# Kernel optimization log

Hardware: AMD Instinct MI355X
Metric: run time of the kernel (lower is better)

## Reference

```python
import jax, jax.numpy as jnp
import numpy as np
import math

B, L, D, H, F = 4, 2048, 1024, 16, 4096
SF = 5          # sampling_factor
EPS = 1e-12     # LayerNorm eps


def setup_inputs() -> dict:
    key = jax.random.key(0)
    ks = jax.random.split(key, 18)
    s = 0.02
    lin = lambda k, i, o: (jax.random.normal(k, (i, o), jnp.float32) * s)
    log_LK = math.ceil(math.log1p(L))
    U_part = min(SF * L * log_LK, L)  # = L here
    return {
        "x": jax.random.normal(ks[0], (B, L, D), jnp.float32),
        "wq": lin(ks[1], D, D), "bq": jnp.zeros((D,), jnp.float32),
        "wk": lin(ks[2], D, D), "bk": jnp.zeros((D,), jnp.float32),
        "wv": lin(ks[3], D, D), "bv": jnp.zeros((D,), jnp.float32),
        "wo": lin(ks[4], D, D), "bo": jnp.zeros((D,), jnp.float32),
        "w1": lin(ks[5], D, F), "b1": jnp.zeros((F,), jnp.float32),
        "w2": lin(ks[6], F, D), "b2": jnp.zeros((D,), jnp.float32),
        "gamma1": jnp.ones((D,), jnp.float32), "beta1": jnp.zeros((D,), jnp.float32),
        "gamma2": jnp.ones((D,), jnp.float32), "beta2": jnp.zeros((D,), jnp.float32),
        "index_sample": jax.random.randint(ks[7], (U_part,), 0, L, jnp.int32),
    }


def _layernorm(x, g, b):
    m = x.mean(-1, keepdims=True)
    v = ((x - m) ** 2).mean(-1, keepdims=True)  # unbiased=False
    return g * (x - m) / jnp.sqrt(v + EPS) + b


def _prob_sparse_mha(x, wq, bq, wk, bk, wv, bv, wo, bo, index_sample):
    d = D // H
    BH = B * H
    # NOTE: source views q as (B, H, L, d) WITHOUT transpose (quirk kept);
    # k, v are split with the usual (B, L, H, d) -> (B, H, L, d) transpose.
    q = (x @ wq + bq).reshape(BH, L, d)
    k = (x @ wk + bk).reshape(B, L, H, d).transpose(0, 2, 1, 3).reshape(BH, L, d)
    v = (x @ wv + bv).reshape(B, L, H, d).transpose(0, 2, 1, 3).reshape(BH, L, d)

    # --- ProbSparse query selection ---
    K_sample = k[:, index_sample, :]                       # [BH, U_part, d]
    QK = jnp.einsum('bqd,bkd->bqk', q, K_sample)           # [BH, L, U_part]
    M = QK.max(axis=-1) - QK.sum(axis=-1) / L              # sparsity measure
    u = min(SF * math.ceil(math.log1p(L)), L)              # static: 40
    _, M_top = jax.lax.top_k(-M, u)                        # largest=False in src
    Q_reduce = jnp.take_along_axis(q, M_top[:, :, None], axis=1)  # [BH, u, d]

    # --- attention for the selected queries ---
    scores = jnp.einsum('bud,bkd->buk', Q_reduce, k) / math.sqrt(d)
    probs = jax.nn.softmax(scores, axis=-1)
    out_red = jnp.einsum('buk,bkd->bud', probs, v)         # [BH, u, d]

    # scatter reduced outputs back to full length (non-selected rows -> 0)
    full = jnp.zeros_like(q).at[jnp.arange(BH)[:, None], M_top].set(out_red)
    out = full.reshape(B, H, L, d).transpose(0, 2, 1, 3).reshape(B, L, D)
    return out @ wo + bo


def reference(x, wq, bq, wk, bk, wv, bv, wo, bo, w1, b1, w2, b2,
              gamma1, beta1, gamma2, beta2, index_sample):
    a = _prob_sparse_mha(x, wq, bq, wk, bk, wv, bv, wo, bo, index_sample)
    x1 = _layernorm(x + a, gamma1, beta1)          # dropout = identity (eval)
    f = jnp.maximum(x1 @ w1 + b1, 0.0) @ w2 + b2   # FFN (ReLU)
    return _layernorm(x1 + f, gamma2, beta2)
```

## Files before the change

### kernel.cpp

```cpp
#include <hip/hip_runtime.h>
#include <float.h>
#include <math.h>

#define L_SEQ 2048
#define D_MODEL 1024
#define N_HEAD 16
#define HD 64
#define N_BH 64
#define U_TOP 40

using bf16x8 = __attribute__((ext_vector_type(8))) short;
using f32x4  = __attribute__((ext_vector_type(4))) float;

__device__ __forceinline__ unsigned short f2bf(float f) {
    unsigned int u = __builtin_bit_cast(unsigned int, f);
    u += 0x7fff + ((u >> 16) & 1);
    return (unsigned short)(u >> 16);
}
__device__ __forceinline__ float bf2f(unsigned short h) {
    unsigned int u = ((unsigned int)h) << 16;
    return __builtin_bit_cast(float, u);
}

__device__ __forceinline__ void gload_lds16(const void* g, void* l) {
    __builtin_amdgcn_global_load_lds(
        (const __attribute__((address_space(1))) unsigned int*)g,
        (__attribute__((address_space(3))) unsigned int*)l, 16, 0, 0);
}

template<bool OUTBF16, bool RELU, bool ACCUM>
__global__ void __launch_bounds__(256)
gemm_bf16(const unsigned short* __restrict__ A, int lda,
          const unsigned short* __restrict__ BT, int ldbt,
          void* __restrict__ Cp, int ldc, int K,
          const float* __restrict__ bias)
{
    __shared__ short As[4096];
    __shared__ short Bs[4096];
    const int tid = threadIdx.x;
    const int w = tid >> 6, l = tid & 63;
    const int bx = blockIdx.x, by = blockIdx.y;
    const int wm = w >> 1, wn = w & 1;

    f32x4 acc[4][4] = {};

    const unsigned short* a_src[2];
    const unsigned short* b_src[2];
#pragma unroll
    for (int g = 0; g < 2; ++g) {
        int r = w * 32 + g * 16 + (l >> 2);
        int kc = (l & 3) ^ ((r >> 1) & 3);
        a_src[g] = A + (size_t)(by * 128 + r) * lda + kc * 8;
        b_src[g] = BT + (size_t)(bx * 128 + r) * ldbt + kc * 8;
    }
    short* As_w = As + w * 1024;
    short* Bs_w = Bs + w * 1024;

    const int lr = l & 15, lg = l >> 4;

    for (int k0 = 0; k0 < K; k0 += 32) {
        __syncthreads();
        gload_lds16(a_src[0] + k0, As_w);
        gload_lds16(a_src[1] + k0, As_w + 512);
        gload_lds16(b_src[0] + k0, Bs_w);
        gload_lds16(b_src[1] + k0, Bs_w + 512);
        __syncthreads();

        bf16x8 af[4], bg[4];
#pragma unroll
        for (int m = 0; m < 4; ++m) {
            int row = wm * 64 + m * 16 + lr;
            int off = row * 64 + ((lg ^ ((row >> 1) & 3)) << 4);
            af[m] = *(const bf16x8*)((const char*)As + off);
        }
#pragma unroll
        for (int n = 0; n < 4; ++n) {
            int row = wn * 64 + n * 16 + lr;
            int off = row * 64 + ((lg ^ ((row >> 1) & 3)) << 4);
            bg[n] = *(const bf16x8*)((const char*)Bs + off);
        }
#pragma unroll
        for (int m = 0; m < 4; ++m)
#pragma unroll
            for (int n = 0; n < 4; ++n)
                acc[m][n] = __builtin_amdgcn_mfma_f32_16x16x32_bf16(
                    af[m], bg[n], acc[m][n], 0, 0, 0);
    }

    float bcol[4];
#pragma unroll
    for (int n = 0; n < 4; ++n) {
        int colg = bx * 128 + wn * 64 + n * 16 + lr;
        bcol[n] = bias ? bias[colg] : 0.f;
    }
#pragma unroll
    for (int m = 0; m < 4; ++m) {
#pragma unroll
        for (int n = 0; n < 4; ++n) {
            int colg = bx * 128 + wn * 64 + n * 16 + lr;
#pragma unroll
            for (int r = 0; r < 4; ++r) {
                int rowg = by * 128 + wm * 64 + m * 16 + lg * 4 + r;
                float v = acc[m][n][r] + bcol[n];
                if (RELU) v = fmaxf(v, 0.f);
                if (OUTBF16) {
                    ((unsigned short*)Cp)[(size_t)rowg * ldc + colg] = f2bf(v);
                } else {
                    float* C = (float*)Cp;
                    if (ACCUM) v += C[(size_t)rowg * ldc + colg];
                    C[(size_t)rowg * ldc + colg] = v;
                }
            }
        }
    }
}

__global__ void __launch_bounds__(256)
gemm_bf16_split(const unsigned short* __restrict__ Ah,
                const unsigned short* __restrict__ Al, int lda,
                const unsigned short* __restrict__ BhT,
                const unsigned short* __restrict__ BlT, int ldbt,
                unsigned short* __restrict__ Ch,
                unsigned short* __restrict__ Cl, int ldc, int K,
                const float* __restrict__ bias)
{
    __shared__ short Ash[4096], Asl[4096], Bsh[4096], Bsl[4096];
    const int tid = threadIdx.x;
    const int w = tid >> 6, l = tid & 63;
    const int bx = blockIdx.x, by = blockIdx.y;
    const int wm = w >> 1, wn = w & 1;

    f32x4 acc[4][4] = {};

    size_t a_off[2], b_off[2];
#pragma unroll
    for (int g = 0; g < 2; ++g) {
        int r = w * 32 + g * 16 + (l >> 2);
        int kc = (l & 3) ^ ((r >> 1) & 3);
        a_off[g] = (size_t)(by * 128 + r) * lda + kc * 8;
        b_off[g] = (size_t)(bx * 128 + r) * ldbt + kc * 8;
    }
    const int wb = w * 1024;
    const int lr = l & 15, lg = l >> 4;

    for (int k0 = 0; k0 < K; k0 += 32) {
        __syncthreads();
#pragma unroll
        for (int g = 0; g < 2; ++g) {
            gload_lds16(Ah + a_off[g] + k0, Ash + wb + g * 512);
            gload_lds16(Al + a_off[g] + k0, Asl + wb + g * 512);
            gload_lds16(BhT + b_off[g] + k0, Bsh + wb + g * 512);
            gload_lds16(BlT + b_off[g] + k0, Bsl + wb + g * 512);
        }
        __syncthreads();

        bf16x8 afh[4], afl[4], bgh[4], bgl[4];
#pragma unroll
        for (int m = 0; m < 4; ++m) {
            int row = wm * 64 + m * 16 + lr;
            int off = row * 64 + ((lg ^ ((row >> 1) & 3)) << 4);
            afh[m] = *(const bf16x8*)((const char*)Ash + off);
            afl[m] = *(const bf16x8*)((const char*)Asl + off);
        }
#pragma unroll
        for (int n = 0; n < 4; ++n) {
            int row = wn * 64 + n * 16 + lr;
            int off = row * 64 + ((lg ^ ((row >> 1) & 3)) << 4);
            bgh[n] = *(const bf16x8*)((const char*)Bsh + off);
            bgl[n] = *(const bf16x8*)((const char*)Bsl + off);
        }
#pragma unroll
        for (int m = 0; m < 4; ++m)
#pragma unroll
            for (int n = 0; n < 4; ++n) {
                acc[m][n] = __builtin_amdgcn_mfma_f32_16x16x32_bf16(
                    afh[m], bgh[n], acc[m][n], 0, 0, 0);
                acc[m][n] = __builtin_amdgcn_mfma_f32_16x16x32_bf16(
                    afh[m], bgl[n], acc[m][n], 0, 0, 0);
                acc[m][n] = __builtin_amdgcn_mfma_f32_16x16x32_bf16(
                    afl[m], bgh[n], acc[m][n], 0, 0, 0);
            }
    }

    float bcol[4];
#pragma unroll
    for (int n = 0; n < 4; ++n)
        bcol[n] = bias[bx * 128 + wn * 64 + n * 16 + lr];
#pragma unroll
    for (int m = 0; m < 4; ++m)
#pragma unroll
        for (int n = 0; n < 4; ++n) {
            int colg = bx * 128 + wn * 64 + n * 16 + lr;
#pragma unroll
            for (int r = 0; r < 4; ++r) {
                int rowg = by * 128 + wm * 64 + m * 16 + lg * 4 + r;
                float v = acc[m][n][r] + bcol[n];
                unsigned short hh = f2bf(v);
                unsigned short ll = f2bf(v - bf2f(hh));
                Ch[(size_t)rowg * ldc + colg] = hh;
                Cl[(size_t)rowg * ldc + colg] = ll;
            }
        }
}

__global__ void __launch_bounds__(256)
mstat_mfma(const unsigned short* __restrict__ Qh, const unsigned short* __restrict__ Ql,
           const unsigned short* __restrict__ Kh, const unsigned short* __restrict__ Kl,
           const int* __restrict__ idxs, float* __restrict__ Mout)
{
    __shared__ short Qs[2][8192];
    __shared__ short Ks[2][4096];
    const int tid = threadIdx.x, w = tid >> 6, l = tid & 63;
    const int itile = blockIdx.x, bh = blockIdx.y;
    const int b = bh >> 4, h = bh & 15;
    const int i0 = itile * 128;
    const int lr = l & 15, lg = l >> 4;

#pragma unroll
    for (int g = w * 4; g < w * 4 + 4; ++g) {
        int row = g * 8 + (l >> 3);
        int kc = (l & 7) ^ (row & 7);
        size_t src = (size_t)(bh * L_SEQ + i0 + row) * HD + kc * 8;
        gload_lds16(Qh + src, (char*)&Qs[0][0] + g * 1024);
        gload_lds16(Ql + src, (char*)&Qs[1][0] + g * 1024);
    }
    __syncthreads();

    bf16x8 af[2][2][2];
#pragma unroll
    for (int m = 0; m < 2; ++m) {
        int row = (w * 2 + m) * 16 + lr;
#pragma unroll
        for (int k = 0; k < 2; ++k) {
            int c = k * 4 + lg;
            int off = row * 128 + ((c ^ (row & 7)) << 4);
            af[m][k][0] = *(const bf16x8*)((const char*)&Qs[0][0] + off);
            af[m][k][1] = *(const bf16x8*)((const char*)&Qs[1][0] + off);
        }
    }

    float mx[2][4], sm[2][4];
#pragma unroll
    for (int m = 0; m < 2; ++m)
#pragma unroll
        for (int r = 0; r < 4; ++r) { mx[m][r] = -FLT_MAX; sm[m][r] = 0.f; }

    for (int jt = 0; jt < 32; ++jt) {
        const int j0 = jt * 64;
        __syncthreads();
#pragma unroll
        for (int g = 2 * w; g <= 2 * w + 1; ++g) {
            int row = g * 8 + (l >> 3);
            int kc = (l & 7) ^ (row & 7);
            int gr = idxs[j0 + row];
            size_t src = (size_t)(b * L_SEQ + gr) * D_MODEL + h * HD + kc * 8;
            gload_lds16(Kh + src, (char*)&Ks[0][0] + g * 1024);
            gload_lds16(Kl + src, (char*)&Ks[1][0] + g * 1024);
        }
        __syncthreads();

        bf16x8 bgh[4][2], bgl[4][2];
#pragma unroll
        for (int n = 0; n < 4; ++n) {
            int row = n * 16 + lr;
#pragma unroll
            for (int k = 0; k < 2; ++k) {
                int c = k * 4 + lg;
                int off = row * 128 + ((c ^ (row & 7)) << 4);
                bgh[n][k] = *(const bf16x8*)((const char*)&Ks[0][0] + off);
                bgl[n][k] = *(const bf16x8*)((const char*)&Ks[1][0] + off);
            }
        }
#pragma unroll
        for (int m = 0; m < 2; ++m) {
            f32x4 a0[4];
#pragma unroll
            for (int n = 0; n < 4; ++n) {
                f32x4 a = {};
                a = __builtin_amdgcn_mfma_f32_16x16x32_bf16(af[m][0][0], bgh[n][0], a, 0, 0, 0);
                a = __builtin_amdgcn_mfma_f32_16x16x32_bf16(af[m][0][0], bgl[n][0], a, 0, 0, 0);
                a = __builtin_amdgcn_mfma_f32_16x16x32_bf16(af[m][0][1], bgh[n][0], a, 0, 0, 0);
                a = __builtin_amdgcn_mfma_f32_16x16x32_bf16(af[m][1][0], bgh[n][1], a, 0, 0, 0);
                a = __builtin_amdgcn_mfma_f32_16x16x32_bf16(af[m][1][0], bgl[n][1], a, 0, 0, 0);
                a = __builtin_amdgcn_mfma_f32_16x16x32_bf16(af[m][1][1], bgh[n][1], a, 0, 0, 0);
                a0[n] = a;
            }
#pragma unroll
            for (int r = 0; r < 4; ++r) {
                float vmax = fmaxf(fmaxf(a0[0][r], a0[1][r]), fmaxf(a0[2][r], a0[3][r]));
                float vsum = (a0[0][r] + a0[1][r]) + (a0[2][r] + a0[3][r]);
                mx[m][r] = fmaxf(mx[m][r], vmax);
                sm[m][r] += vsum;
            }
        }
    }

#pragma unroll
    for (int m = 0; m < 2; ++m)
#pragma unroll
        for (int r = 0; r < 4; ++r) {
            float a = mx[m][r], s = sm[m][r];
#pragma unroll
            for (int mask = 1; mask < 16; mask <<= 1) {
                a = fmaxf(a, __shfl_xor(a, mask));
                s += __shfl_xor(s, mask);
            }
            if (lr == 0) {
                int row = i0 + (w * 2 + m) * 16 + lg * 4 + r;
                Mout[(size_t)bh * L_SEQ + row] = a - s * (1.0f / 2048.0f);
            }
        }
}

__global__ void __launch_bounds__(256)
tconv(const float* __restrict__ in, int R, int C, unsigned short* __restrict__ out)
{
    __shared__ float t[32][33];
    const int bx = blockIdx.x * 32;
    const int by = blockIdx.y * 32;
    const int lx = threadIdx.x & 31, ly = threadIdx.x >> 5;
#pragma unroll
    for (int r = 0; r < 4; ++r)
        t[ly + r * 8][lx] = in[(size_t)(by + ly + r * 8) * C + bx + lx];
    __syncthreads();
#pragma unroll
    for (int r = 0; r < 4; ++r) {
        int oc = ly + r * 8;
        out[(size_t)(bx + oc) * R + by + lx] = f2bf(t[lx][oc]);
    }
}

__global__ void __launch_bounds__(256)
tconv_split(const float* __restrict__ in, int R, int C,
            unsigned short* __restrict__ outh, unsigned short* __restrict__ outl)
{
    __shared__ float t[32][33];
    const int bx = blockIdx.x * 32;
    const int by = blockIdx.y * 32;
    const int lx = threadIdx.x & 31, ly = threadIdx.x >> 5;
#pragma unroll
    for (int r = 0; r < 4; ++r)
        t[ly + r * 8][lx] = in[(size_t)(by + ly + r * 8) * C + bx + lx];
    __syncthreads();
#pragma unroll
    for (int r = 0; r < 4; ++r) {
        int oc = ly + r * 8;
        float f = t[lx][oc];
        unsigned short hh = f2bf(f);
        outh[(size_t)(bx + oc) * R + by + lx] = hh;
        outl[(size_t)(bx + oc) * R + by + lx] = f2bf(f - bf2f(hh));
    }
}

__global__ void __launch_bounds__(256)
split_f32(const float* __restrict__ in, unsigned short* __restrict__ hi,
          unsigned short* __restrict__ lo)
{
    size_t i = ((size_t)blockIdx.x * 256 + threadIdx.x) * 4;
    float4 v = *(const float4*)(in + i);
    ushort4 h, l2;
    h.x = f2bf(v.x); l2.x = f2bf(v.x - bf2f(h.x));
    h.y = f2bf(v.y); l2.y = f2bf(v.y - bf2f(h.y));
    h.z = f2bf(v.z); l2.z = f2bf(v.z - bf2f(h.z));
    h.w = f2bf(v.w); l2.w = f2bf(v.w - bf2f(h.w));
    *(ushort4*)(hi + i) = h;
    *(ushort4*)(lo + i) = l2;
}

__global__ void __launch_bounds__(256)
topk_kernel(const float* __restrict__ M, int* __restrict__ Mtop)
{
    __shared__ float mv[L_SEQ];
    __shared__ float wv_[4];
    __shared__ int wi_[4];
    const int bh = blockIdx.x;
    const int tid = threadIdx.x;
    for (int j = tid; j < L_SEQ; j += 256) mv[j] = M[(size_t)bh * L_SEQ + j];
    __syncthreads();
    for (int u = 0; u < U_TOP; ++u) {
        float best = FLT_MAX;
        int bi = 1 << 30;
        for (int j = tid; j < L_SEQ; j += 256) {
            float v = mv[j];
            if (v < best || (v == best && j < bi)) { best = v; bi = j; }
        }
#pragma unroll
        for (int off = 32; off; off >>= 1) {
            float ov = __shfl_down(best, off);
            int oi = __shfl_down(bi, off);
            if (ov < best || (ov == best && oi < bi)) { best = ov; bi = oi; }
        }
        if ((tid & 63) == 0) { wv_[tid >> 6] = best; wi_[tid >> 6] = bi; }
        __syncthreads();
        if (tid == 0) {
            for (int w = 1; w < 4; ++w)
                if (wv_[w] < best || (wv_[w] == best && wi_[w] < bi)) { best = wv_[w]; bi = wi_[w]; }
            Mtop[bh * U_TOP + u] = bi;
            mv[bi] = FLT_MAX;
        }
        __syncthreads();
    }
}

__global__ void __launch_bounds__(256)
attn_fused(const unsigned short* __restrict__ Q,
           const unsigned short* __restrict__ K,
           const unsigned short* __restrict__ V,
           const int* __restrict__ Mtop,
           unsigned short* __restrict__ ATT)
{
    __shared__ unsigned short Qs[64 * 64];
    __shared__ unsigned short Ks[128 * 64];
    __shared__ unsigned short Vt[64 * 128];
    __shared__ unsigned short Pb[64 * 128];
    const int bh = blockIdx.x;
    const int b = bh >> 4, h = bh & 15;
    const int tid = threadIdx.x, w = tid >> 6, l = tid & 63;
    const int lr = l & 15, lg = l >> 4;

#pragma unroll
    for (int is = 0; is < 2; ++is) {
        int row = w * 16 + is * 8 + (l >> 3);
        int u = row < U_TOP ? row : U_TOP - 1;
        int lsel = Mtop[bh * U_TOP + u];
        int cg = (l & 7) ^ (row & 7);
        gload_lds16(Q + (((size_t)(bh * L_SEQ + lsel)) << 6) + cg * 8,
                    &Qs[(w * 16 + is * 8) * 64]);
    }
    __syncthreads();

    bf16x8 af[2];
    {
        int row = w * 16 + lr;
#pragma unroll
        for (int ks = 0; ks < 2; ++ks) {
            int c = (ks * 4 + lg) ^ (row & 7);
            af[ks] = *(const bf16x8*)((const char*)Qs + row * 128 + (c << 4));
        }
    }

    float m_run[4], l_run[4];
    f32x4 oacc[4] = {};
#pragma unroll
    for (int r = 0; r < 4; ++r) { m_run[r] = -FLT_MAX; l_run[r] = 0.f; }

    for (int t = 0; t < 16; ++t) {
        const int j0 = t * 128;
        __syncthreads();

#pragma unroll
        for (int is = 0; is < 4; ++is) {
            int kr = w * 32 + is * 8 + (l >> 3);
            int cg = (l & 7) ^ (kr & 7);
            gload_lds16(K + (((size_t)(b * L_SEQ + j0 + kr)) << 10) + (h << 6) + cg * 8,
                        &Ks[(w * 32 + is * 8) * 64]);
        }
        {
            int key = tid & 127, dh = (tid >> 7) * 32;
            const unsigned short* vsrc =
                V + (((size_t)(b * L_SEQ + j0 + key)) << 10) + (h << 6) + dh;
            bf16x8 vv[4];
#pragma unroll
            for (int i = 0; i < 4; ++i) vv[i] = *(const bf16x8*)(vsrc + i * 8);
            int ck = key >> 3, klo = (key & 7) * 2;
#pragma unroll
            for (int i = 0; i < 4; ++i)
#pragma unroll
                for (int j = 0; j < 8; ++j) {
                    int d = dh + i * 8 + j;
                    *(unsigned short*)((char*)Vt + d * 256 +
                                       ((ck ^ (d & 7)) << 4) + klo) =
                        (unsigned short)vv[i][j];
                }
        }
        __syncthreads();

        f32x4 sc[8] = {};
#pragma unroll
        for (int ks = 0; ks < 2; ++ks)
#pragma unroll
            for (int n = 0; n < 8; ++n) {
                int krow = n * 16 + lr;
                int c = (ks * 4 + lg) ^ (krow & 7);
                bf16x8 bf = *(const bf16x8*)((const char*)Ks + krow * 128 + (c << 4));
                sc[n] = __builtin_amdgcn_mfma_f32_16x16x32_bf16(af[ks], bf, sc[n], 0, 0, 0);
            }

        float rs[4];
#pragma unroll
        for (int r = 0; r < 4; ++r) {
            int row = w * 16 + lg * 4 + r;
            float mt = -FLT_MAX;
#pragma unroll
            for (int n = 0; n < 8; ++n) mt = fmaxf(mt, sc[n][r]);
            mt *= 0.125f;
#pragma unroll
            for (int mask = 1; mask < 16; mask <<= 1)
                mt = fmaxf(mt, __shfl_xor(mt, mask));
            float mn = fmaxf(m_run[r], mt);
            rs[r] = expf(m_run[r] - mn);
            float ls = 0.f;
            int rsw = row & 7;
#pragma unroll
            for (int n = 0; n < 8; ++n) {
                float p = expf(sc[n][r] * 0.125f - mn);
                ls += p;
                int ckp = (lr >> 3) + 2 * n;
                *(unsigned short*)((char*)Pb + row * 256 +
                                   ((ckp ^ rsw) << 4) + (lr & 7) * 2) = f2bf(p);
            }
#pragma unroll
            for (int mask = 1; mask < 16; mask <<= 1) ls += __shfl_xor(ls, mask);
            l_run[r] = l_run[r] * rs[r] + ls;
            m_run[r] = mn;
        }
        __syncthreads();

#pragma unroll
        for (int n = 0; n < 4; ++n)
#pragma unroll
            for (int r = 0; r < 4; ++r) oacc[n][r] *= rs[r];
#pragma unroll
        for (int ks = 0; ks < 4; ++ks) {
            int arow = w * 16 + lr;
            int ca = (lg + ks * 4) ^ (arow & 7);
            bf16x8 pa = *(const bf16x8*)((const char*)Pb + arow * 256 + (ca << 4));
#pragma unroll
            for (int n = 0; n < 4; ++n) {
                int d = n * 16 + lr;
                int cb = (lg + ks * 4) ^ (d & 7);
                bf16x8 vb = *(const bf16x8*)((const char*)Vt + d * 256 + (cb << 4));
                oacc[n] = __builtin_amdgcn_mfma_f32_16x16x32_bf16(pa, vb, oacc[n], 0, 0, 0);
            }
        }
    }

#pragma unroll
    for (int r = 0; r < 4; ++r) {
        int row = w * 16 + lg * 4 + r;
        if (row < U_TOP) {
            int lsel = Mtop[bh * U_TOP + row];
            float inv = 1.f / l_run[r];
            size_t base = (((size_t)(b * L_SEQ + lsel)) << 10) + (h << 6);
#pragma unroll
            for (int n = 0; n < 4; ++n)
                ATT[base + n * 16 + lr] = f2bf(oacc[n][r] * inv);
        }
    }
}

template<bool WB16>
__global__ void __launch_bounds__(256)
ln_kernel(const float* __restrict__ X, const float* __restrict__ A,
          const float* __restrict__ g, const float* __restrict__ be,
          float* __restrict__ out, unsigned short* __restrict__ out16)
{
    __shared__ float wred[4];
    const int row = blockIdx.x, tid = threadIdx.x;
    float4 xv = *(const float4*)(X + (size_t)row * D_MODEL + tid * 4);
    float4 av = *(const float4*)(A + (size_t)row * D_MODEL + tid * 4);
    float v0 = xv.x + av.x, v1 = xv.y + av.y, v2 = xv.z + av.z, v3 = xv.w + av.w;

    float s = v0 + v1 + v2 + v3;
#pragma unroll
    for (int off = 32; off; off >>= 1) s += __shfl_down(s, off);
    if ((tid & 63) == 0) wred[tid >> 6] = s;
    __syncthreads();
    float mean = (wred[0] + wred[1] + wred[2] + wred[3]) * (1.f / 1024.f);
    __syncthreads();

    float d0 = v0 - mean, d1 = v1 - mean, d2 = v2 - mean, d3 = v3 - mean;
    float q = d0 * d0 + d1 * d1 + d2 * d2 + d3 * d3;
#pragma unroll
    for (int off = 32; off; off >>= 1) q += __shfl_down(q, off);
    if ((tid & 63) == 0) wred[tid >> 6] = q;
    __syncthreads();
    float var = (wred[0] + wred[1] + wred[2] + wred[3]) * (1.f / 1024.f);
    float rstd = rsqrtf(var + 1e-12f);

    float4 gv = *(const float4*)(g + tid * 4);
    float4 bv = *(const float4*)(be + tid * 4);
    float4 o;
    o.x = gv.x * d0 * rstd + bv.x;
    o.y = gv.y * d1 * rstd + bv.y;
    o.z = gv.z * d2 * rstd + bv.z;
    o.w = gv.w * d3 * rstd + bv.w;
    *(float4*)(out + (size_t)row * D_MODEL + tid * 4) = o;
    if (WB16) {
        ushort4 ob;
        ob.x = f2bf(o.x); ob.y = f2bf(o.y); ob.z = f2bf(o.z); ob.w = f2bf(o.w);
        *(ushort4*)(out16 + (size_t)row * D_MODEL + tid * 4) = ob;
    }
}

extern "C" void kernel_launch(void* const* d_in, const int* in_sizes, int n_in,
                              void* d_out, int out_size, void* d_ws, size_t ws_size,
                              hipStream_t stream)
{
    const float* x   = (const float*)d_in[0];
    const float* wq  = (const float*)d_in[1];
    const float* bq  = (const float*)d_in[2];
    const float* wk  = (const float*)d_in[3];
    const float* bk  = (const float*)d_in[4];
    const float* wv  = (const float*)d_in[5];
    const float* bv  = (const float*)d_in[6];
    const float* wo  = (const float*)d_in[7];
    const float* bo  = (const float*)d_in[8];
    const float* w1  = (const float*)d_in[9];
    const float* b1  = (const float*)d_in[10];
    const float* w2  = (const float*)d_in[11];
    const float* b2  = (const float*)d_in[12];
    const float* g1  = (const float*)d_in[13];
    const float* be1 = (const float*)d_in[14];
    const float* g2  = (const float*)d_in[15];
    const float* be2 = (const float*)d_in[16];
    const int*  idxs = (const int*)d_in[17];

    char* ws = (char*)d_ws;
    const size_t MB = 1u << 20;
    unsigned short* Qhb  = (unsigned short*)(ws);
    unsigned short* Qlb  = (unsigned short*)(ws + 16 * MB);
    unsigned short* Khb  = (unsigned short*)(ws + 32 * MB);
    unsigned short* Klb  = (unsigned short*)(ws + 48 * MB);
    unsigned short* xh   = (unsigned short*)(ws + 64 * MB);
    unsigned short* xl   = (unsigned short*)(ws + 80 * MB);
    unsigned short* ATTb = (unsigned short*)(ws + 64 * MB);
    unsigned short* x1b  = (unsigned short*)(ws + 80 * MB);
    unsigned short* wqhT = (unsigned short*)(ws + 96 * MB);
    unsigned short* wqlT = (unsigned short*)(ws + 98 * MB);
    unsigned short* wkhT = (unsigned short*)(ws + 100 * MB);
    unsigned short* wklT = (unsigned short*)(ws + 102 * MB);
    unsigned short* wvT  = (unsigned short*)(ws + 104 * MB);
    unsigned short* woT  = (unsigned short*)(ws + 106 * MB);
    float* Mb            = (float*)(ws + 96 * MB);
    int*   Mtop          = (int*)(ws + 97 * MB);
    unsigned short* Vb   = (unsigned short*)(ws + 108 * MB);
    float* Ab            = (float*)(ws);
    float* x1f           = (float*)(ws + 32 * MB);
    unsigned short* w1T  = (unsigned short*)(ws + 96 * MB);
    unsigned short* w2T  = (unsigned short*)(ws + 104 * MB);
    unsigned short* HIDc = (unsigned short*)(ws);
    float* F             = (float*)d_out;

    dim3 blk(256);
    dim3 g_gemm(8, 64);

    split_f32<<<dim3(8192), blk, 0, stream>>>(x, xh, xl);
    tconv_split<<<dim3(32, 32), blk, 0, stream>>>(wq, 1024, 1024, wqhT, wqlT);
    tconv_split<<<dim3(32, 32), blk, 0, stream>>>(wk, 1024, 1024, wkhT, wklT);
    tconv<<<dim3(32, 32), blk, 0, stream>>>(wv, 1024, 1024, wvT);
    tconv<<<dim3(32, 32), blk, 0, stream>>>(wo, 1024, 1024, woT);

    gemm_bf16_split<<<g_gemm, blk, 0, stream>>>(xh, xl, 1024, wqhT, wqlT, 1024,
                                                Qhb, Qlb, 1024, 1024, bq);
    gemm_bf16_split<<<g_gemm, blk, 0, stream>>>(xh, xl, 1024, wkhT, wklT, 1024,
                                                Khb, Klb, 1024, 1024, bk);
    gemm_bf16<true, false, false><<<g_gemm, blk, 0, stream>>>(xh, 1024, wvT, 1024,
                                                              Vb, 1024, 1024, bv);

    mstat_mfma<<<dim3(16, 64), blk, 0, stream>>>(Qhb, Qlb, Khb, Klb, idxs, Mb);
    topk_kernel<<<dim3(64), blk, 0, stream>>>(Mb, Mtop);

    hipMemsetAsync(ATTb, 0, 16 * MB, stream);
    attn_fused<<<dim3(N_BH), blk, 0, stream>>>(Qhb, Khb, Vb, Mtop, ATTb);

    gemm_bf16<false, false, false><<<g_gemm, blk, 0, stream>>>(ATTb, 1024, woT, 1024,
                                                               Ab, 1024, 1024, bo);
    ln_kernel<true><<<dim3(8192), blk, 0, stream>>>(x, Ab, g1, be1, x1f, x1b);

    tconv<<<dim3(128, 32), blk, 0, stream>>>(w1, 1024, 4096, w1T);
    tconv<<<dim3(32, 128), blk, 0, stream>>>(w2, 4096, 1024, w2T);

    for (int c = 0; c < 2; ++c) {
        gemm_bf16<true, true, false><<<dim3(16, 64), blk, 0, stream>>>(
            x1b, 1024, w1T + (size_t)c * 2048 * 1024, 1024, HIDc, 2048, 1024, b1 + c * 2048);
        if (c == 0)
            gemm_bf16<false, false, false><<<g_gemm, blk, 0, stream>>>(
                HIDc, 2048, w2T + c * 2048, 4096, F, 1024, 2048, b2);
        else
            gemm_bf16<false, false, true><<<g_gemm, blk, 0, stream>>>(
                HIDc, 2048, w2T + c * 2048, 4096, F, 1024, 2048, nullptr);
    }

    ln_kernel<false><<<dim3(8192), blk, 0, stream>>>(x1f, F, g2, be2, (float*)d_out, nullptr);
}
```

Before: 862.1 us.

## Exploit sparse attention output: scatter-project via Wo, pack Q/K hi-lo, pre-gather K samples

Replaces the dense attention-output GEMM with a small kernel that multiplies only the 40 selected rows per head by the Wo slice and atomically adds into a zeroed buffer, with the bias moved into the LayerNorm. This skips a full 8192x1024x1024 GEMM on mostly-zero rows. Q and K hi/lo halves are now interleaved in one packed layout, and the sampled K rows are gathered once into a contiguous buffer so the M-statistic kernel can double-buffer plain loads with larger query tiles. Atomics make the summation order nondeterministic, and several buffers now live in the output region.

```diff
diff --git a/kernel.cpp b/kernel.cpp
--- a/kernel.cpp
+++ b/kernel.cpp
@@ -120,8 +120,7 @@
                 const unsigned short* __restrict__ Al, int lda,
                 const unsigned short* __restrict__ BhT,
                 const unsigned short* __restrict__ BlT, int ldbt,
-                unsigned short* __restrict__ Ch,
-                unsigned short* __restrict__ Cl, int ldc, int K,
+                unsigned short* __restrict__ CP, int K,
                 const float* __restrict__ bias)
 {
     __shared__ short Ash[4096], Asl[4096], Bsh[4096], Bsl[4096];
@@ -186,117 +185,134 @@
 #pragma unroll
     for (int n = 0; n < 4; ++n)
         bcol[n] = bias[bx * 128 + wn * 64 + n * 16 + lr];
+    const int cg = bx * 2 + wn;
 #pragma unroll
     for (int m = 0; m < 4; ++m)
 #pragma unroll
         for (int n = 0; n < 4; ++n) {
-            int colg = bx * 128 + wn * 64 + n * 16 + lr;
+            int cwi = n * 16 + lr;
 #pragma unroll
             for (int r = 0; r < 4; ++r) {
                 int rowg = by * 128 + wm * 64 + m * 16 + lg * 4 + r;
                 float v = acc[m][n][r] + bcol[n];
                 unsigned short hh = f2bf(v);
                 unsigned short ll = f2bf(v - bf2f(hh));
-                Ch[(size_t)rowg * ldc + colg] = hh;
-                Cl[(size_t)rowg * ldc + colg] = ll;
-            }
-        }
-}
-
-__global__ void __launch_bounds__(256)
-mstat_mfma(const unsigned short* __restrict__ Qh, const unsigned short* __restrict__ Ql,
-           const unsigned short* __restrict__ Kh, const unsigned short* __restrict__ Kl,
-           const int* __restrict__ idxs, float* __restrict__ Mout)
-{
-    __shared__ short Qs[2][8192];
-    __shared__ short Ks[2][4096];
+                size_t ad = (size_t)rowg * 2048 + cg * 128 + cwi;
+                CP[ad] = hh;
+                CP[ad + 64] = ll;
+            }
+        }
+}
+
+__global__ void __launch_bounds__(256)
+gather_ks(const unsigned short* __restrict__ KP, const int* __restrict__ idxs,
+          unsigned short* __restrict__ KS)
+{
+    const int bh = blockIdx.x, b = bh >> 4, h = bh & 15;
+    const int r0 = blockIdx.y * 256;
+    const int s = threadIdx.x & 15, jr = threadIdx.x >> 4;
+#pragma unroll
+    for (int p = 0; p < 16; ++p) {
+        int j = r0 + p * 16 + jr;
+        int idx = idxs[j];
+        int kc = (s & 7) ^ (j & 7);
+        const unsigned short* src = KP + (size_t)(b * 2048 + idx) * 2048
+                                  + h * 128 + ((s & 8) << 3) + kc * 8;
+        *(bf16x8*)(KS + ((size_t)bh * 2048 + j) * 128 + s * 8) =
+            *(const bf16x8*)src;
+    }
+}
+
+__global__ void __launch_bounds__(256)
+mstat_mfma2(const unsigned short* __restrict__ QP,
+            const unsigned short* __restrict__ KS,
+            float* __restrict__ Mout)
+{
+    __shared__ char lds[32768];
     const int tid = threadIdx.x, w = tid >> 6, l = tid & 63;
-    const int itile = blockIdx.x, bh = blockIdx.y;
-    const int b = bh >> 4, h = bh & 15;
-    const int i0 = itile * 128;
+    const int bh = blockIdx.x, qt = blockIdx.y;
+    const int i0 = qt * 256;
     const int lr = l & 15, lg = l >> 4;
 
-#pragma unroll
-    for (int g = w * 4; g < w * 4 + 4; ++g) {
-        int row = g * 8 + (l >> 3);
-        int kc = (l & 7) ^ (row & 7);
-        size_t src = (size_t)(bh * L_SEQ + i0 + row) * HD + kc * 8;
-        gload_lds16(Qh + src, (char*)&Qs[0][0] + g * 1024);
-        gload_lds16(Ql + src, (char*)&Qs[1][0] + g * 1024);
+    bf16x8 af[4][2][2];
+#pragma unroll
+    for (int half = 0; half < 2; ++half) {
+        __syncthreads();
+#pragma unroll
+        for (int it = 0; it < 8; ++it) {
+            int rq = w * 64 + it * 8 + (l >> 3);
+            int i = i0 + rq;
+            int kc = (l & 7) ^ (rq & 7);
+            gload_lds16(QP + (size_t)(bh * 128 + (i >> 4)) * 2048
+                           + (i & 15) * 128 + half * 64 + kc * 8,
+                        lds + w * 8192 + it * 1024);
+        }
+        __syncthreads();
+#pragma unroll
+        for (int m = 0; m < 4; ++m) {
+            int rq = w * 64 + m * 16 + lr;
+#pragma unroll
+            for (int ks = 0; ks < 2; ++ks) {
+                int c = (ks * 4 + lg) ^ (rq & 7);
+                af[m][ks][half] = *(const bf16x8*)(lds + rq * 128 + (c << 4));
+            }
+        }
     }
     __syncthreads();
 
-    bf16x8 af[2][2][2];
-#pragma unroll
-    for (int m = 0; m < 2; ++m) {
-        int row = (w * 2 + m) * 16 + lr;
-#pragma unroll
-        for (int k = 0; k < 2; ++k) {
-            int c = k * 4 + lg;
-            int off = row * 128 + ((c ^ (row & 7)) << 4);
-            af[m][k][0] = *(const bf16x8*)((const char*)&Qs[0][0] + off);
-            af[m][k][1] = *(const bf16x8*)((const char*)&Qs[1][0] + off);
-        }
-    }
-
-    float mx[2][4], sm[2][4];
-#pragma unroll
-    for (int m = 0; m < 2; ++m)
+    float mx[4][4], sm[4][4];
+#pragma unroll
+    for (int m = 0; m < 4; ++m)
 #pragma unroll
         for (int r = 0; r < 4; ++r) { mx[m][r] = -FLT_MAX; sm[m][r] = 0.f; }
 
+    const unsigned short* ksbase = KS + (size_t)bh * (2048 * 128);
+
+#pragma unroll
+    for (int it = 0; it < 4; ++it)
+        gload_lds16(ksbase + w * 2048 + it * 512 + l * 8,
+                    lds + w * 4096 + it * 1024);
+
     for (int jt = 0; jt < 32; ++jt) {
-        const int j0 = jt * 64;
-        __syncthreads();
-#pragma unroll
-        for (int g = 2 * w; g <= 2 * w + 1; ++g) {
-            int row = g * 8 + (l >> 3);
-            int kc = (l & 7) ^ (row & 7);
-            int gr = idxs[j0 + row];
-            size_t src = (size_t)(b * L_SEQ + gr) * D_MODEL + h * HD + kc * 8;
-            gload_lds16(Kh + src, (char*)&Ks[0][0] + g * 1024);
-            gload_lds16(Kl + src, (char*)&Ks[1][0] + g * 1024);
-        }
-        __syncthreads();
-
-        bf16x8 bgh[4][2], bgl[4][2];
+        const int cur = jt & 1;
+        __syncthreads();
+        if (jt + 1 < 32) {
+#pragma unroll
+            for (int it = 0; it < 4; ++it)
+                gload_lds16(ksbase + (size_t)(jt + 1) * 8192 + w * 2048 + it * 512 + l * 8,
+                            lds + (cur ^ 1) * 16384 + w * 4096 + it * 1024);
+        }
+        const char* kb = lds + cur * 16384;
 #pragma unroll
         for (int n = 0; n < 4; ++n) {
-            int row = n * 16 + lr;
-#pragma unroll
-            for (int k = 0; k < 2; ++k) {
-                int c = k * 4 + lg;
-                int off = row * 128 + ((c ^ (row & 7)) << 4);
-                bgh[n][k] = *(const bf16x8*)((const char*)&Ks[0][0] + off);
-                bgl[n][k] = *(const bf16x8*)((const char*)&Ks[1][0] + off);
-            }
-        }
-#pragma unroll
-        for (int m = 0; m < 2; ++m) {
-            f32x4 a0[4];
-#pragma unroll
-            for (int n = 0; n < 4; ++n) {
+            int jr = n * 16 + lr;
+            bf16x8 bgh[2], bgl[2];
+#pragma unroll
+            for (int ks = 0; ks < 2; ++ks) {
+                int c = (ks * 4 + lg) ^ (jr & 7);
+                bgh[ks] = *(const bf16x8*)(kb + jr * 256 + (c << 4));
+                bgl[ks] = *(const bf16x8*)(kb + jr * 256 + (c << 4) + 128);
+            }
+#pragma unroll
+            for (int m = 0; m < 4; ++m) {
                 f32x4 a = {};
-                a = __builtin_amdgcn_mfma_f32_16x16x32_bf16(af[m][0][0], bgh[n][0], a, 0, 0, 0);
-                a = __builtin_amdgcn_mfma_f32_16x16x32_bf16(af[m][0][0], bgl[n][0], a, 0, 0, 0);
-                a = __builtin_amdgcn_mfma_f32_16x16x32_bf16(af[m][0][1], bgh[n][0], a, 0, 0, 0);
-                a = __builtin_amdgcn_mfma_f32_16x16x32_bf16(af[m][1][0], bgh[n][1], a, 0, 0, 0);
-                a = __builtin_amdgcn_mfma_f32_16x16x32_bf16(af[m][1][0], bgl[n][1], a, 0, 0, 0);
-                a = __builtin_amdgcn_mfma_f32_16x16x32_bf16(af[m][1][1], bgh[n][1], a, 0, 0, 0);
-                a0[n] = a;
-            }
-#pragma unroll
-            for (int r = 0; r < 4; ++r) {
-                float vmax = fmaxf(fmaxf(a0[0][r], a0[1][r]), fmaxf(a0[2][r], a0[3][r]));
-                float vsum = (a0[0][r] + a0[1][r]) + (a0[2][r] + a0[3][r]);
-                mx[m][r] = fmaxf(mx[m][r], vmax);
-                sm[m][r] += vsum;
-            }
-        }
-    }
-
-#pragma unroll
-    for (int m = 0; m < 2; ++m)
+                a = __builtin_amdgcn_mfma_f32_16x16x32_bf16(af[m][0][0], bgh[0], a, 0, 0, 0);
+                a = __builtin_amdgcn_mfma_f32_16x16x32_bf16(af[m][0][1], bgh[0], a, 0, 0, 0);
+                a = __builtin_amdgcn_mfma_f32_16x16x32_bf16(af[m][0][0], bgl[0], a, 0, 0, 0);
+                a = __builtin_amdgcn_mfma_f32_16x16x32_bf16(af[m][1][0], bgh[1], a, 0, 0, 0);
+                a = __builtin_amdgcn_mfma_f32_16x16x32_bf16(af[m][1][1], bgh[1], a, 0, 0, 0);
+                a = __builtin_amdgcn_mfma_f32_16x16x32_bf16(af[m][1][0], bgl[1], a, 0, 0, 0);
+#pragma unroll
+                for (int r = 0; r < 4; ++r) {
+                    mx[m][r] = fmaxf(mx[m][r], a[r]);
+                    sm[m][r] += a[r];
+                }
+            }
+        }
+    }
+
+#pragma unroll
+    for (int m = 0; m < 4; ++m)
 #pragma unroll
         for (int r = 0; r < 4; ++r) {
             float a = mx[m][r], s = sm[m][r];
@@ -306,7 +322,7 @@
                 s += __shfl_xor(s, mask);
             }
             if (lr == 0) {
-                int row = i0 + (w * 2 + m) * 16 + lg * 4 + r;
+                int row = i0 + w * 64 + m * 16 + lg * 4 + r;
                 Mout[(size_t)bh * L_SEQ + row] = a - s * (1.0f / 2048.0f);
             }
         }
@@ -403,11 +419,11 @@
 }
 
 __global__ void __launch_bounds__(256)
-attn_fused(const unsigned short* __restrict__ Q,
-           const unsigned short* __restrict__ K,
+attn_fused(const unsigned short* __restrict__ QP,
+           const unsigned short* __restrict__ KP,
            const unsigned short* __restrict__ V,
            const int* __restrict__ Mtop,
-           unsigned short* __restrict__ ATT)
+           unsigned short* __restrict__ OUTC)
 {
     __shared__ unsigned short Qs[64 * 64];
     __shared__ unsigned short Ks[128 * 64];
@@ -424,7 +440,8 @@
         int u = row < U_TOP ? row : U_TOP - 1;
         int lsel = Mtop[bh * U_TOP + u];
         int cg = (l & 7) ^ (row & 7);
-        gload_lds16(Q + (((size_t)(bh * L_SEQ + lsel)) << 6) + cg * 8,
+        gload_lds16(QP + (size_t)(bh * 128 + (lsel >> 4)) * 2048
+                       + (lsel & 15) * 128 + cg * 8,
                     &Qs[(w * 16 + is * 8) * 64]);
     }
     __syncthreads();
@@ -452,7 +469,7 @@
         for (int is = 0; is < 4; ++is) {
             int kr = w * 32 + is * 8 + (l >> 3);
             int cg = (l & 7) ^ (kr & 7);
-            gload_lds16(K + (((size_t)(b * L_SEQ + j0 + kr)) << 10) + (h << 6) + cg * 8,
+            gload_lds16(KP + (size_t)(b * 2048 + j0 + kr) * 2048 + h * 128 + cg * 8,
                         &Ks[(w * 32 + is * 8) * 64]);
         }
         {
@@ -538,20 +555,66 @@
 #pragma unroll
     for (int r = 0; r < 4; ++r) {
         int row = w * 16 + lg * 4 + r;
-        if (row < U_TOP) {
-            int lsel = Mtop[bh * U_TOP + row];
-            float inv = 1.f / l_run[r];
-            size_t base = (((size_t)(b * L_SEQ + lsel)) << 10) + (h << 6);
-#pragma unroll
-            for (int n = 0; n < 4; ++n)
-                ATT[base + n * 16 + lr] = f2bf(oacc[n][r] * inv);
-        }
-    }
-}
-
-template<bool WB16>
+        float inv = 1.f / l_run[r];
+#pragma unroll
+        for (int n = 0; n < 4; ++n)
+            OUTC[bh * 4096 + row * 64 + n * 16 + lr] = f2bf(oacc[n][r] * inv);
+    }
+}
+
+__global__ void __launch_bounds__(256)
+woscatter(const unsigned short* __restrict__ OUTC,
+          const unsigned short* __restrict__ woT,
+          const int* __restrict__ Mtop,
+          float* __restrict__ Ab)
+{
+    const int bh = blockIdx.x, b = bh >> 4, h = bh & 15;
+    const int tid = threadIdx.x, w = tid >> 6, l = tid & 63;
+    const int lr = l & 15, lg = l >> 4;
+
+    bf16x8 af[3][2];
+#pragma unroll
+    for (int m = 0; m < 3; ++m)
+#pragma unroll
+        for (int ks = 0; ks < 2; ++ks)
+            af[m][ks] = *(const bf16x8*)(OUTC + bh * 4096 + (m * 16 + lr) * 64
+                                         + (ks * 4 + lg) * 8);
+    int lsel[3][4];
+#pragma unroll
+    for (int m = 0; m < 3; ++m)
+#pragma unroll
+        for (int r = 0; r < 4; ++r) {
+            int row = m * 16 + lg * 4 + r;
+            lsel[m][r] = row < U_TOP ? Mtop[bh * U_TOP + row] : -1;
+        }
+
+    for (int nn = 0; nn < 16; ++nn) {
+        int ng = w * 16 + nn;
+        bf16x8 bg[2];
+#pragma unroll
+        for (int ks = 0; ks < 2; ++ks)
+            bg[ks] = *(const bf16x8*)(woT + (size_t)(ng * 16 + lr) * 1024
+                                      + h * 64 + (ks * 4 + lg) * 8);
+        f32x4 a[3] = {};
+#pragma unroll
+        for (int m = 0; m < 3; ++m)
+#pragma unroll
+            for (int ks = 0; ks < 2; ++ks)
+                a[m] = __builtin_amdgcn_mfma_f32_16x16x32_bf16(af[m][ks], bg[ks], a[m], 0, 0, 0);
+#pragma unroll
+        for (int m = 0; m < 3; ++m)
+#pragma unroll
+            for (int r = 0; r < 4; ++r)
+                if (lsel[m][r] >= 0)
+                    atomicAdd(Ab + (size_t)(b * 2048 + lsel[m][r]) * 1024
+                              + ng * 16 + lr, a[m][r]);
+    }
+}
+
+template<bool WB16, bool BADD>
 __global__ void __launch_bounds__(256)
 ln_kernel(const float* __restrict__ X, const float* __restrict__ A,
+          const float* __restrict__ badd,
           const float* __restrict__ g, const float* __restrict__ be,
           float* __restrict__ out, unsigned short* __restrict__ out16)
 {
@@ -560,6 +623,10 @@
     float4 xv = *(const float4*)(X + (size_t)row * D_MODEL + tid * 4);
     float4 av = *(const float4*)(A + (size_t)row * D_MODEL + tid * 4);
     float v0 = xv.x + av.x, v1 = xv.y + av.y, v2 = xv.z + av.z, v3 = xv.w + av.w;
+    if (BADD) {
+        float4 bb = *(const float4*)(badd + tid * 4);
+        v0 += bb.x; v1 += bb.y; v2 += bb.z; v3 += bb.w;
+    }
 
     float s = v0 + v1 + v2 + v3;
 #pragma unroll
@@ -616,31 +683,33 @@
     const float* be2 = (const float*)d_in[16];
     const int*  idxs = (const int*)d_in[17];
 
-    char* ws = (char*)d_ws;
+    char* ws  = (char*)d_ws;
+    char* dob = (char*)d_out;
     const size_t MB = 1u << 20;
-    unsigned short* Qhb  = (unsigned short*)(ws);
-    unsigned short* Qlb  = (unsigned short*)(ws + 16 * MB);
-    unsigned short* Khb  = (unsigned short*)(ws + 32 * MB);
-    unsigned short* Klb  = (unsigned short*)(ws + 48 * MB);
+
+    unsigned short* QP   = (unsigned short*)(ws);
+    unsigned short* KP   = (unsigned short*)(ws + 32 * MB);
     unsigned short* xh   = (unsigned short*)(ws + 64 * MB);
     unsigned short* xl   = (unsigned short*)(ws + 80 * MB);
-    unsigned short* ATTb = (unsigned short*)(ws + 64 * MB);
-    unsigned short* x1b  = (unsigned short*)(ws + 80 * MB);
-    unsigned short* wqhT = (unsigned short*)(ws + 96 * MB);
-    unsigned short* wqlT = (unsigned short*)(ws + 98 * MB);
-    unsigned short* wkhT = (unsigned short*)(ws + 100 * MB);
-    unsigned short* wklT = (unsigned short*)(ws + 102 * MB);
-    unsigned short* wvT  = (unsigned short*)(ws + 104 * MB);
-    unsigned short* woT  = (unsigned short*)(ws + 106 * MB);
-    float* Mb            = (float*)(ws + 96 * MB);
-    int*   Mtop          = (int*)(ws + 97 * MB);
-    unsigned short* Vb   = (unsigned short*)(ws + 108 * MB);
-    float* Ab            = (float*)(ws);
-    float* x1f           = (float*)(ws + 32 * MB);
-    unsigned short* w1T  = (unsigned short*)(ws + 96 * MB);
-    unsigned short* w2T  = (unsigned short*)(ws + 104 * MB);
-    unsigned short* HIDc = (unsigned short*)(ws);
-    float* F             = (float*)d_out;
+    unsigned short* KS   = (unsigned short*)(ws + 64 * MB);
+    float*          Ab   = (float*)(ws + 64 * MB);
+    float*          x1f  = (float*)(ws + 96 * MB);
+    unsigned short* x1b  = (unsigned short*)(ws);
+    unsigned short* w1T  = (unsigned short*)(ws + 16 * MB);
+    unsigned short* w2T  = (unsigned short*)(ws + 24 * MB);
+    unsigned short* HIDc = (unsigned short*)(ws + 32 * MB);
+
+    unsigned short* woT  = (unsigned short*)(dob);
+    unsigned short* wqhT = (unsigned short*)(dob + 2 * MB);
+    unsigned short* wqlT = (unsigned short*)(dob + 4 * MB);
+    unsigned short* wkhT = (unsigned short*)(dob + 6 * MB);
+    unsigned short* wklT = (unsigned short*)(dob + 8 * MB);
+    unsigned short* wvT  = (unsigned short*)(dob + 10 * MB);
+    float*          Mb   = (float*)(dob + 12 * MB);
+    int*            Mtop = (int*)(dob + 12 * MB + 768 * 1024);
+    unsigned short* Vb   = (unsigned short*)(dob + 13 * MB);
+    unsigned short* OUTC = (unsigned short*)(dob + 29 * MB);
+    float*          F    = (float*)d_out;
 
     dim3 blk(256);
     dim3 g_gemm(8, 64);
@@ -652,21 +721,21 @@
     tconv<<<dim3(32, 32), blk, 0, stream>>>(wo, 1024, 1024, woT);
 
     gemm_bf16_split<<<g_gemm, blk, 0, stream>>>(xh, xl, 1024, wqhT, wqlT, 1024,
-                                                Qhb, Qlb, 1024, 1024, bq);
+                                                QP, 1024, bq);
     gemm_bf16_split<<<g_gemm, blk, 0, stream>>>(xh, xl, 1024, wkhT, wklT, 1024,
-                                                Khb, Klb, 1024, 1024, bk);
+                                                KP, 1024, bk);
     gemm_bf16<true, false, false><<<g_gemm, blk, 0, stream>>>(xh, 1024, wvT, 1024,
                                                               Vb, 1024, 1024, bv);
 
-    mstat_mfma<<<dim3(16, 64), blk, 0, stream>>>(Qhb, Qlb, Khb, Klb, idxs, Mb);
+    gather_ks<<<dim3(64, 8), blk, 0, stream>>>(KP, idxs, KS);
+    mstat_mfma2<<<dim3(64, 8), blk, 0, stream>>>(QP, KS, Mb);
     topk_kernel<<<dim3(64), blk, 0, stream>>>(Mb, Mtop);
 
-    hipMemsetAsync(ATTb, 0, 16 * MB, stream);
-    attn_fused<<<dim3(N_BH), blk, 0, stream>>>(Qhb, Khb, Vb, Mtop, ATTb);
-
-    gemm_bf16<false, false, false><<<g_gemm, blk, 0, stream>>>(ATTb, 1024, woT, 1024,
-                                                               Ab, 1024, 1024, bo);
-    ln_kernel<true><<<dim3(8192), blk, 0, stream>>>(x, Ab, g1, be1, x1f, x1b);
+    hipMemsetAsync(Ab, 0, 32 * MB, stream);
+    attn_fused<<<dim3(N_BH), blk, 0, stream>>>(QP, KP, Vb, Mtop, OUTC);
+    woscatter<<<dim3(N_BH), blk, 0, stream>>>(OUTC, woT, Mtop, Ab);
+
+    ln_kernel<true, true><<<dim3(8192), blk, 0, stream>>>(x, Ab, bo, g1, be1, x1f, x1b);
 
     tconv<<<dim3(128, 32), blk, 0, stream>>>(w1, 1024, 4096, w1T);
     tconv<<<dim3(32, 128), blk, 0, stream>>>(w2, 4096, 1024, w2T);
@@ -682,5 +751,6 @@
                 HIDc, 2048, w2T + c * 2048, 4096, F, 1024, 2048, nullptr);
     }
 
-    ln_kernel<false><<<dim3(8192), blk, 0, stream>>>(x1f, F, g2, be2, (float*)d_out, nullptr);
-}
+    ln_kernel<false, false><<<dim3(8192), blk, 0, stream>>>(x1f, F, nullptr, g2, be2,
+                                                            (float*)d_out, nullptr);
+}
```

Result: faster. 840.0 us (-2.6%).
